# Performance work log

Hardware: AMD Instinct MI355X
Metric: run time of the kernel (lower is better)

The kernel has to match this reference:

```python
import jax, jax.numpy as jnp
import numpy as np

B, T, DIM = 4, 1024, 1024
HEADS, DH = 16, 64
MEM, CMEM, RATIO = 1024, 256, 4
KV = CMEM + MEM + T  # 2304
TOTAL_MEM = MEM + CMEM  # 1280
NEG = -np.finfo(np.float32).max


def shift(x):
    # Faithful port of the pad/flatten/reshape relative-position shift trick.
    b, h, i, j = x.shape
    x = jnp.concatenate([x, jnp.zeros((b, h, i, i), x.dtype)], axis=-1)  # [b,h,i,i+j]
    l = i + j - 1
    x = x.reshape(b, h, i * (i + j))
    pad = (-x.shape[-1]) % l
    x = jnp.pad(x, ((0, 0), (0, 0), (0, pad)))
    x = x.reshape(b, h, -1, l)
    return x[:, :, :i, i - 1:]  # [b,h,i,j]


def setup_inputs() -> dict:
    key = jax.random.key(0)
    ks = jax.random.split(key, 10)
    s = 0.02
    return {
        "x": jax.random.normal(ks[0], (B, T, DIM), jnp.float32),
        "mem": jax.random.normal(ks[1], (B, MEM, DIM), jnp.float32),
        "cmem": jax.random.normal(ks[2], (B, CMEM, DIM), jnp.float32),
        "pos_emb": jax.random.normal(ks[3], (HEADS, KV, DH), jnp.float32),
        "input_mask": jnp.ones((B, T), bool),
        "Wq": jax.random.normal(ks[4], (DIM, DIM), jnp.float32) * s,
        "Wkv": jax.random.normal(ks[5], (2 * DIM, DIM), jnp.float32) * s,
        "Wout": jax.random.normal(ks[6], (DIM, DIM), jnp.float32) * s,
        "bout": jnp.zeros((DIM,), jnp.float32),
        "conv_w": jax.random.normal(ks[7], (DIM, DIM, RATIO), jnp.float32) * s,
        "conv_b": jnp.zeros((DIM,), jnp.float32),
    }


def reference(x, mem, cmem, pos_emb, input_mask, Wq, Wkv, Wout, bout, conv_w, conv_b):
    b, t, e = x.shape
    scale = DH ** -0.5

    q = x @ Wq.T                                             # [b,t,e]
    kv_input = jnp.concatenate([cmem, mem, x], axis=1)       # [b,kv,e]
    kv_len = kv_input.shape[1]
    kv = kv_input @ Wkv.T                                    # [b,kv,2e]
    k, v = jnp.split(kv, 2, axis=-1)

    def mh(z):
        return z.reshape(z.shape[0], z.shape[1], HEADS, DH).transpose(0, 2, 1, 3)

    qh, kh, vh = mh(q), mh(k), mh(v)                         # [b,h,*,dh]

    dots = jnp.einsum('bhid,bhjd->bhij', qh, kh) * scale     # [b,h,t,kv]

    pe = pos_emb[:, -kv_len:].astype(qh.dtype)               # [h,kv,dh]
    pos_dots = shift(jnp.einsum('bhid,hjd->bhij', qh, pe) * scale)
    dots = dots + pos_dots

    # input mask (padded True over mem+cmem positions)
    m = input_mask[:, None, :, None] & input_mask[:, None, None, :]  # [b,1,t,t]
    m = jnp.pad(m, ((0, 0), (0, 0), (0, 0), (TOTAL_MEM, 0)), constant_values=True)
    dots = jnp.where(m, dots, NEG)

    # causal mask shifted by total memory length
    causal = jnp.triu(jnp.ones((t, t + TOTAL_MEM), bool), k=1 + TOTAL_MEM)
    dots = jnp.where(causal[None, None], NEG, dots)

    attn = jax.nn.softmax(dots, axis=-1)
    out = jnp.einsum('bhij,bhjd->bhid', attn, vh)
    out = out.transpose(0, 2, 1, 3).reshape(b, t, e)
    logits = out @ Wout.T + bout

    # memory update (eval path, calc_memory=True)
    queue = jnp.concatenate([mem, x], axis=1)                # [b,mem+t,e]
    new_mem = queue[:, -MEM:]
    old_mem = jax.lax.stop_gradient(queue[:, :-MEM])         # [b,t,e], t % RATIO == 0
    comp = jax.lax.conv_general_dilated(
        old_mem.transpose(0, 2, 1), conv_w, (RATIO,), 'VALID',
        dimension_numbers=('NCH', 'OIH', 'NCH')) + conv_b[None, :, None]
    comp = comp.transpose(0, 2, 1)                           # [b,t//RATIO,e]
    new_cmem = jnp.concatenate([cmem, comp], axis=1)[:, -CMEM:]

    return logits, new_mem, new_cmem
```

## Files before the change

### kernel.cpp

```cpp
#include <hip/hip_runtime.h>
#include <hip/hip_bf16.h>
#include <hip/hip_fp16.h>
#include <cstdint>
#include <cstddef>
#include <cstring>

using bf16 = __hip_bfloat16;

constexpr int TS    = 1024;
constexpr int DIM   = 1024;
constexpr int MEMN  = 1024;
constexpr int CMEMN = 256;
constexpr int KVN   = 2304;
constexpr int TMEM  = 1280;

typedef __attribute__((ext_vector_type(8))) short short8;
typedef __attribute__((ext_vector_type(4))) float f32x4;

__device__ __forceinline__ unsigned short f2bf_us(float f){
    __hip_bfloat16 t = __float2bfloat16(f);
    unsigned short us; memcpy(&us, &t, 2); return us;
}
__device__ __forceinline__ int sw8(int row){ return (row & 7) ^ ((row >> 3) & 7); }

__device__ __forceinline__ short8 ldfrag(const unsigned short* base, int row, int chunk) {
    int ch = chunk ^ sw8(row);
    return *(const short8*)(base + row*64 + ch*8);
}
__device__ __forceinline__ void gl2lds16(const void* g, void* l) {
    __builtin_amdgcn_global_load_lds(
        (const __attribute__((address_space(1))) void*)g,
        (__attribute__((address_space(3))) void*)l, 16, 0, 0);
}
__device__ __forceinline__ short8 ldg8(const unsigned short* p){ return *(const short8*)p; }

__global__ __launch_bounds__(256) void pack(
    const float* __restrict__ x, const float* __restrict__ memp,
    const float* __restrict__ cmem, const float* __restrict__ Wq,
    const float* __restrict__ Wkv, const float* __restrict__ Wout,
    const float* __restrict__ cw, const float* __restrict__ pe,
    unsigned short* __restrict__ kvin, unsigned short* __restrict__ wqb,
    unsigned short* __restrict__ wkvb, unsigned short* __restrict__ woutb,
    unsigned short* __restrict__ cw2b, unsigned short* __restrict__ peb)
{
    const size_t t8 = ((size_t)blockIdx.x * 256 + threadIdx.x) * 8;
    unsigned short h[8];
    if (t8 < 9437184) {
        size_t g = t8 >> 10;
        int cc = (int)(t8 & 1023);
        int b = (int)(g / KVN), j = (int)(g % KVN);
        const float* src;
        if (j < CMEMN)      src = cmem + ((size_t)b*CMEMN + j)*1024 + cc;
        else if (j < TMEM)  src = memp + ((size_t)b*MEMN + (j - CMEMN))*1024 + cc;
        else                src = x    + ((size_t)b*TS   + (j - TMEM))*1024 + cc;
        float4 f0 = *(const float4*)src; float4 f1 = *(const float4*)(src + 4);
        h[0]=f2bf_us(f0.x); h[1]=f2bf_us(f0.y); h[2]=f2bf_us(f0.z); h[3]=f2bf_us(f0.w);
        h[4]=f2bf_us(f1.x); h[5]=f2bf_us(f1.y); h[6]=f2bf_us(f1.z); h[7]=f2bf_us(f1.w);
        *(uint4*)(kvin + t8) = *(const uint4*)h;
    } else if (t8 < 13631488) {
        const float* src; unsigned short* dst; float sc = 1.0f;
        if (t8 < 10485760)      { src = Wq   + (t8 - 9437184);  dst = wqb   + (t8 - 9437184); sc = 0.125f; }
        else if (t8 < 12582912) { src = Wkv  + (t8 - 10485760); dst = wkvb  + (t8 - 10485760); }
        else                    { src = Wout + (t8 - 12582912); dst = woutb + (t8 - 12582912); }
        float4 f0 = *(const float4*)src; float4 f1 = *(const float4*)(src + 4);
        h[0]=f2bf_us(f0.x*sc); h[1]=f2bf_us(f0.y*sc); h[2]=f2bf_us(f0.z*sc); h[3]=f2bf_us(f0.w*sc);
        h[4]=f2bf_us(f1.x*sc); h[5]=f2bf_us(f1.y*sc); h[6]=f2bf_us(f1.z*sc); h[7]=f2bf_us(f1.w*sc);
        *(uint4*)dst = *(const uint4*)h;
    } else if (t8 < 17825792) {
        size_t o8 = t8 - 13631488;
        int o = (int)(o8 >> 12); int rem = (int)(o8 & 4095);
        int r = rem >> 10, i = rem & 1023;
        #pragma unroll
        for (int p = 0; p < 8; ++p) h[p] = f2bf_us(cw[(o << 12) + (i + p)*4 + r]);
        *(uint4*)(cw2b + o8) = *(const uint4*)h;
    } else {
        size_t o8 = t8 - 17825792;
        const float* src = pe + o8;
        float4 f0 = *(const float4*)src; float4 f1 = *(const float4*)(src + 4);
        h[0]=f2bf_us(f0.x); h[1]=f2bf_us(f0.y); h[2]=f2bf_us(f0.z); h[3]=f2bf_us(f0.w);
        h[4]=f2bf_us(f1.x); h[5]=f2bf_us(f1.y); h[6]=f2bf_us(f1.z); h[7]=f2bf_us(f1.w);
        *(uint4*)(peb + o8) = *(const uint4*)h;
    }
}

template<int EPI, int QMODE>
__global__ __launch_bounds__(256) void gemm_mfma(
    const bf16* __restrict__ Abf, const bf16* __restrict__ Bbf,
    const float* __restrict__ bias, void* __restrict__ Cptr,
    void* __restrict__ C2, int M, int N, int K)
{
    __shared__ alignas(16) unsigned short As[128*64];
    __shared__ alignas(16) unsigned short Bs[128*64];
    const int tid = threadIdx.x, lane = tid & 63, w = tid >> 6;
    const int quad = lane >> 4, colq = lane & 15;
    const int wm = w >> 1, wn = w & 1;
    const int m0 = blockIdx.x * 128, n0 = blockIdx.y * 128;
    size_t abase;
    if (QMODE == 0)      abase = (size_t)m0 * K;
    else if (QMODE == 1) abase = ((size_t)((m0 >> 10)*KVN + TMEM + (m0 & 1023))) * 1024;
    else                 abase = ((size_t)((m0 >> 8)*KVN + CMEMN)) * 1024 + (size_t)(m0 & 255) * 4096;
    const unsigned short* Ag = (const unsigned short*)Abf + abase;
    const unsigned short* Bg = (const unsigned short*)Bbf + (size_t)n0 * K;

    const int srow0 = w*32 + (lane >> 3);
    const int sch2  = lane & 7;

    f32x4 acc[4][4];
    #pragma unroll
    for (int i = 0; i < 4; ++i)
        #pragma unroll
        for (int j = 0; j < 4; ++j) acc[i][j] = (f32x4){0.f,0.f,0.f,0.f};

    for (int k0 = 0; k0 < K; k0 += 64) {
        __syncthreads();
        #pragma unroll
        for (int c = 0; c < 4; ++c) {
            int rr = srow0 + c*8;
            int ch = sch2 ^ sw8(rr);
            gl2lds16(Ag + (size_t)rr*K + k0 + ch*8, &As[(w*32 + c*8)*64]);
            gl2lds16(Bg + (size_t)rr*K + k0 + ch*8, &Bs[(w*32 + c*8)*64]);
        }
        __syncthreads();
        short8 af[4][2], bfr[4][2];
        #pragma unroll
        for (int i = 0; i < 4; ++i) {
            af[i][0]  = ldfrag(As, wm*64 + i*16 + colq, quad);
            af[i][1]  = ldfrag(As, wm*64 + i*16 + colq, 4 + quad);
            bfr[i][0] = ldfrag(Bs, wn*64 + i*16 + colq, quad);
            bfr[i][1] = ldfrag(Bs, wn*64 + i*16 + colq, 4 + quad);
        }
        #pragma unroll
        for (int i = 0; i < 4; ++i)
            #pragma unroll
            for (int j = 0; j < 4; ++j) {
                f32x4 t = __builtin_amdgcn_mfma_f32_16x16x32_bf16(af[i][0], bfr[j][0], acc[i][j], 0, 0, 0);
                acc[i][j] = __builtin_amdgcn_mfma_f32_16x16x32_bf16(af[i][1], bfr[j][1], t, 0, 0, 0);
            }
    }
    if (EPI == 2) {
        const int b = m0 / KVN;
        const int jj0 = (m0 - b*KVN) + wm*64;
        if (n0 < 1024) {
            bf16* kn = (bf16*)Cptr;
            #pragma unroll
            for (int j = 0; j < 4; ++j) {
                int col = n0 + wn*64 + j*16 + colq;
                #pragma unroll
                for (int i = 0; i < 4; ++i)
                    #pragma unroll
                    for (int r = 0; r < 4; ++r)
                        kn[(size_t)(b*KVN + jj0 + i*16 + quad*4 + r)*1024 + col] =
                            __float2bfloat16(acc[i][j][r]);
            }
        } else {
            unsigned short* vp = (unsigned short*)C2;
            #pragma unroll
            for (int j = 0; j < 4; ++j) {
                int col = n0 + wn*64 + j*16 + colq;
                int hh = (col >> 6) & 15, d = col & 63;
                #pragma unroll
                for (int i = 0; i < 4; ++i) {
                    int jjb = jj0 + i*16 + quad*4;
                    ushort4 u;
                    u.x = f2bf_us(acc[i][j][0]); u.y = f2bf_us(acc[i][j][1]);
                    u.z = f2bf_us(acc[i][j][2]); u.w = f2bf_us(acc[i][j][3]);
                    *(ushort4*)(vp + ((size_t)((b*16 + hh)*64 + d))*KVN + jjb) = u;
                }
            }
        }
    } else {
        #pragma unroll
        for (int j = 0; j < 4; ++j) {
            int col = n0 + wn*64 + j*16 + colq;
            float bj = bias ? bias[col] : 0.0f;
            #pragma unroll
            for (int i = 0; i < 4; ++i)
                #pragma unroll
                for (int r = 0; r < 4; ++r) {
                    size_t row = (size_t)(m0 + wm*64 + i*16 + quad*4 + r);
                    float v = acc[i][j][r] + bj;
                    if (EPI == 1) ((bf16*)Cptr)[row*N + col] = __float2bfloat16(v);
                    else          ((float*)Cptr)[row*N + col] = v;
                }
        }
    }
}

__global__ __launch_bounds__(256, 2) void attn(
    const unsigned short* __restrict__ qg,
    const unsigned short* __restrict__ kq,
    const unsigned short* __restrict__ vh,
    const unsigned short* __restrict__ peb,
    bf16* __restrict__ out)
{
    __shared__ alignas(16) unsigned short Kt[64*64];
    __shared__ alignas(16) unsigned short Vt[64*64];
    __shared__ alignas(16) unsigned short PEr[256*64];
    __shared__ alignas(16) unsigned short Pb[128*64];

    const int tid  = threadIdx.x;
    const int lane = tid & 63, w = tid >> 6;
    const int quad = lane >> 4, colq = lane & 15;
    const int jr = lane >> 3, l7 = lane & 7;

    const int bx = blockIdx.x;
    const int b = bx & 3, h = (bx >> 2) & 15, q0 = (bx >> 6) * 128;

    #pragma unroll
    for (int c = 0; c < 4; ++c) {
        int row = c*32 + w*8 + jr;
        gl2lds16(qg + ((size_t)(b*1024 + q0 + row))*1024 + h*64 + (l7 ^ sw8(row))*8,
                 &Pb[(c*32 + w*8)*64]);
    }
    const int c0p = 896 - q0;
    #pragma unroll
    for (int c = 0; c < 4; ++c) {
        int cg = c0p + c*32 + w*8 + jr;
        int slot = cg & 255;
        gl2lds16(peb + ((size_t)h*KVN + cg)*64 + (l7 ^ sw8(slot))*8,
                 &PEr[((c0p + c*32 + w*8) & 255)*64]);
    }
    __syncthreads();
    short8 qa[2][2];
    #pragma unroll
    for (int it2 = 0; it2 < 2; ++it2) {
        qa[it2][0] = ldfrag(Pb, 32*w + 16*it2 + colq, quad);
        qa[it2][1] = ldfrag(Pb, 32*w + 16*it2 + colq, 4 + quad);
    }

    const unsigned short* kbase = kq  + (size_t)b*KVN*1024 + h*64;
    const unsigned short* vbase = vh  + ((size_t)((b*16 + h)*64))*KVN;
    const unsigned short* pbase = peb + (size_t)h*KVN*64;

    const int row0 = w*8 + jr, row1 = 32 + w*8 + jr;
    const int ch0 = (l7 ^ sw8(row0))*8;
    const int ch1 = (l7 ^ sw8(row1))*8;

    f32x4 oacc[2][4];
    float l_[2][4];
    #pragma unroll
    for (int it2 = 0; it2 < 2; ++it2) {
        #pragma unroll
        for (int dt = 0; dt < 4; ++dt) oacc[it2][dt] = (f32x4){0.f,0.f,0.f,0.f};
        #pragma unroll
        for (int r = 0; r < 4; ++r) l_[it2][r] = 0.f;
    }
    const f32x4 zero4 = (f32x4){0.f,0.f,0.f,0.f};
    const int nkv = min(36, ((q0 + 1407) >> 6) + 1);

    short8 kr0, kr1, vr0, vr1, pr0, pr1;
    {
        kr0 = ldg8(kbase + (size_t)(row0)*1024 + ch0);
        kr1 = ldg8(kbase + (size_t)(row1)*1024 + ch1);
        vr0 = ldg8(vbase + (size_t)row0*KVN + ch0);
        vr1 = ldg8(vbase + (size_t)row1*KVN + ch1);
        int cb = 0 - q0 + 1024;
        int cg0 = cb + row0, cg1 = cb + row1;
        pr0 = ldg8(pbase + (size_t)min(cg0, KVN-1)*64 + ch0);
        pr1 = ldg8(pbase + (size_t)min(cg1, KVN-1)*64 + ch1);
    }

    for (int kvt = 0; kvt < nkv; ++kvt) {
        const int kv0 = kvt * 64;
        asm volatile("s_waitcnt lgkmcnt(0)" ::: "memory");
        __builtin_amdgcn_s_barrier();
        *(short8*)(&Kt[row0*64 + l7*8]) = kr0;
        *(short8*)(&Kt[row1*64 + l7*8]) = kr1;
        *(short8*)(&Vt[row0*64 + l7*8]) = vr0;
        *(short8*)(&Vt[row1*64 + l7*8]) = vr1;
        {
            int cb = kv0 - q0 + 1024;
            int s0 = (cb + row0) & 255, s1 = (cb + row1) & 255;
            *(short8*)(&PEr[s0*64 + l7*8]) = pr0;
            *(short8*)(&PEr[s1*64 + l7*8]) = pr1;
        }
        if (kvt + 1 < nkv) {
            int kvn = kv0 + 64;
            kr0 = ldg8(kbase + (size_t)(kvn + row0)*1024 + ch0);
            kr1 = ldg8(kbase + (size_t)(kvn + row1)*1024 + ch1);
            vr0 = ldg8(vbase + (size_t)row0*KVN + kvn + ch0);
            vr1 = ldg8(vbase + (size_t)row1*KVN + kvn + ch1);
            int cb2 = kvn - q0 + 1024;
            int cg0 = cb2 + row0, cg1 = cb2 + row1;
            pr0 = ldg8(pbase + (size_t)min(cg0, KVN-1)*64 + ch0);
            pr1 = ldg8(pbase + (size_t)min(cg1, KVN-1)*64 + ch1);
        }
        __builtin_amdgcn_sched_barrier(0);
        asm volatile("s_waitcnt lgkmcnt(0)" ::: "memory");
        __builtin_amdgcn_s_barrier();

        short8 kf[4][2], vf[4][2];
        #pragma unroll
        for (int nt = 0; nt < 4; ++nt) {
            kf[nt][0] = ldfrag(Kt, nt*16 + colq, quad);
            kf[nt][1] = ldfrag(Kt, nt*16 + colq, 4 + quad);
            vf[nt][0] = ldfrag(Vt, nt*16 + colq, quad);
            vf[nt][1] = ldfrag(Vt, nt*16 + colq, 4 + quad);
        }

        #pragma unroll
        for (int it2 = 0; it2 < 2; ++it2) {
            f32x4 facc[4];
            __builtin_amdgcn_s_setprio(1);
            #pragma unroll
            for (int nt = 0; nt < 4; ++nt) {
                f32x4 t = __builtin_amdgcn_mfma_f32_16x16x32_bf16(qa[it2][0], kf[nt][0], zero4, 0, 0, 0);
                facc[nt] = __builtin_amdgcn_mfma_f32_16x16x32_bf16(qa[it2][1], kf[nt][1], t, 0, 0, 0);
            }
            const int cb = kv0 - q0 + 1008 - 32*w - 16*it2;
            f32x4 pacc[5];
            #pragma unroll
            for (int pnt = 0; pnt < 5; ++pnt) {
                int slot = (cb + pnt*16 + colq) & 255;
                short8 b0 = ldfrag(PEr, slot, quad);
                short8 b1 = ldfrag(PEr, slot, 4 + quad);
                f32x4 t = __builtin_amdgcn_mfma_f32_16x16x32_bf16(qa[it2][0], b0, zero4, 0, 0, 0);
                pacc[pnt] = __builtin_amdgcn_mfma_f32_16x16x32_bf16(qa[it2][1], b1, t, 0, 0, 0);
            }
            __builtin_amdgcn_s_setprio(0);
            const int prow0 = 32*w + 16*it2 + 4*quad;
            #pragma unroll
            for (int r = 0; r < 4; ++r) {
                int tt = colq + 15 - 4*quad - r;
                int src = (lane & 48) | (tt & 15);
                float sh[5];
                #pragma unroll
                for (int p = 0; p < 5; ++p) sh[p] = __shfl(pacc[p][r], src, 64);
                int ig = q0 + prow0 + r;
                float lsum = 0.f;
                float ps[4];
                #pragma unroll
                for (int nt = 0; nt < 4; ++nt) {
                    float g = (tt < 16) ? sh[nt] : sh[nt + 1];
                    float v = facc[nt][r] + g;
                    int jg = kv0 + nt*16 + colq;
                    float s = (jg - ig > TMEM) ? -1e30f : v;
                    ps[nt] = __expf(s);
                    lsum += ps[nt];
                }
                l_[it2][r] += lsum;
                int prow = prow0 + r;
                int swp = sw8(prow);
                #pragma unroll
                for (int nt = 0; nt < 4; ++nt) {
                    int cc = nt*16 + colq;
                    Pb[prow*64 + (((cc >> 3) ^ swp))*8 + (cc & 7)] = f2bf_us(ps[nt]);
                }
            }
            short8 pa0 = ldfrag(Pb, 32*w + 16*it2 + colq, quad);
            short8 pa1 = ldfrag(Pb, 32*w + 16*it2 + colq, 4 + quad);
            __builtin_amdgcn_s_setprio(1);
            #pragma unroll
            for (int dt = 0; dt < 4; ++dt) {
                f32x4 t = __builtin_amdgcn_mfma_f32_16x16x32_bf16(pa0, vf[dt][0], oacc[it2][dt], 0, 0, 0);
                oacc[it2][dt] = __builtin_amdgcn_mfma_f32_16x16x32_bf16(pa1, vf[dt][1], t, 0, 0, 0);
            }
            __builtin_amdgcn_s_setprio(0);
        }
    }

    #pragma unroll
    for (int it2 = 0; it2 < 2; ++it2) {
        #pragma unroll
        for (int r = 0; r < 4; ++r) {
            float lt = l_[it2][r];
            #pragma unroll
            for (int off = 1; off < 16; off <<= 1) lt += __shfl_xor(lt, off, 64);
            float inv = 1.0f / lt;
            size_t row = (size_t)(b*1024 + q0 + 32*w + 16*it2 + 4*quad + r);
            #pragma unroll
            for (int dt = 0; dt < 4; ++dt)
                out[row*1024 + h*64 + dt*16 + colq] = __float2bfloat16(oacc[it2][dt][r] * inv);
        }
    }
}

__global__ __launch_bounds__(256) void copy_u4(const uint4* __restrict__ src,
                                               uint4* __restrict__ dst, int n)
{
    int i = blockIdx.x * 256 + threadIdx.x;
    if (i < n) dst[i] = src[i];
}

extern "C" void kernel_launch(void* const* d_in, const int* in_sizes, int n_in,
                              void* d_out, int out_size, void* d_ws, size_t ws_size,
                              hipStream_t stream)
{
    const float* x    = (const float*)d_in[0];
    const float* memp = (const float*)d_in[1];
    const float* cmem = (const float*)d_in[2];
    const float* pe   = (const float*)d_in[3];
    const float* Wq   = (const float*)d_in[5];
    const float* Wkv  = (const float*)d_in[6];
    const float* Wout = (const float*)d_in[7];
    const float* bout = (const float*)d_in[8];
    const float* cw   = (const float*)d_in[9];
    const float* cb   = (const float*)d_in[10];
    float* outp = (float*)d_out;

    char* wsb = (char*)d_ws;
    unsigned short* kvin  = (unsigned short*)(wsb);
    unsigned short* knat  = (unsigned short*)(wsb + 18874368);
    unsigned short* vhb   = (unsigned short*)(wsb + 37748736);
    unsigned short* qb    = (unsigned short*)(wsb + 56623104);
    bf16*           ao    = (bf16*)(wsb + 65011712);
    unsigned short* wqb   = (unsigned short*)(wsb + 73400320);
    unsigned short* wkvb  = (unsigned short*)(wsb + 75497472);
    unsigned short* woutb = (unsigned short*)(wsb + 79691776);
    unsigned short* cw2b  = (unsigned short*)(wsb + 81788928);
    unsigned short* peb   = (unsigned short*)(wsb + 90177536);

    pack<<<dim3(9856), 256, 0, stream>>>(x, memp, cmem, Wq, Wkv, Wout, cw, pe,
        kvin, wqb, wkvb, woutb, cw2b, peb);
    gemm_mfma<1,1><<<dim3(32, 8), 256, 0, stream>>>((const bf16*)kvin, (const bf16*)wqb,
        nullptr, qb, nullptr, 4096, 1024, 1024);
    gemm_mfma<2,0><<<dim3(72, 16), 256, 0, stream>>>((const bf16*)kvin, (const bf16*)wkvb,
        nullptr, knat, vhb, 9216, 2048, 1024);
    attn<<<dim3(512), 256, 0, stream>>>(qb, knat, vhb, peb, ao);
    gemm_mfma<0,0><<<dim3(32, 8), 256, 0, stream>>>(ao, (const bf16*)woutb,
        bout, outp, nullptr, 4096, 1024, 1024);
    copy_u4<<<dim3(4096), 256, 0, stream>>>((const uint4*)x,
        (uint4*)(outp + 4194304), 1048576);
    gemm_mfma<0,2><<<dim3(8, 8), 256, 0, stream>>>((const bf16*)kvin, (const bf16*)cw2b,
        cb, outp + 8388608, nullptr, 1024, 1024, 4096);
}
```

Measured before the change: 583.5 us.

## Double-buffer K/V via direct global-to-LDS loads and use exp2 softmax

The attention kernel now stages K, V and positional-embedding tiles straight into LDS with async global-to-LDS loads into a two-deep K/V buffer, replacing the register-staged copy. Two tiles are kept in flight and synchronised with vmcnt waits. Q fragments are loaded straight from global into registers. The softmax uses exp2 with log2(e) folded into the Wq prescale, and QK and PE MFMAs for both row groups are batched before the softmax. The Pb scratch is halved. Risks are vmcnt accounting errors, and a possible correctness problem because Pb rows are now indexed as 16*w+4*quad for both it2 iterations, so the two passes reuse the same rows.

```diff
diff --git a/kernel.cpp b/kernel.cpp
--- a/kernel.cpp
+++ b/kernel.cpp
@@ -59,7 +59,7 @@
         *(uint4*)(kvin + t8) = *(const uint4*)h;
     } else if (t8 < 13631488) {
         const float* src; unsigned short* dst; float sc = 1.0f;
-        if (t8 < 10485760)      { src = Wq   + (t8 - 9437184);  dst = wqb   + (t8 - 9437184); sc = 0.125f; }
+        if (t8 < 10485760)      { src = Wq   + (t8 - 9437184);  dst = wqb   + (t8 - 9437184); sc = 0.18033688011112043f; }
         else if (t8 < 12582912) { src = Wkv  + (t8 - 10485760); dst = wkvb  + (t8 - 10485760); }
         else                    { src = Wout + (t8 - 12582912); dst = woutb + (t8 - 12582912); }
         float4 f0 = *(const float4*)src; float4 f1 = *(const float4*)(src + 4);
@@ -193,10 +193,10 @@
     const unsigned short* __restrict__ peb,
     bf16* __restrict__ out)
 {
-    __shared__ alignas(16) unsigned short Kt[64*64];
-    __shared__ alignas(16) unsigned short Vt[64*64];
+    __shared__ alignas(16) unsigned short Kt[2][64*64];
+    __shared__ alignas(16) unsigned short Vt[2][64*64];
     __shared__ alignas(16) unsigned short PEr[256*64];
-    __shared__ alignas(16) unsigned short Pb[128*64];
+    __shared__ alignas(16) unsigned short Pb[64*64];
 
     const int tid  = threadIdx.x;
     const int lane = tid & 63, w = tid >> 6;
@@ -206,35 +206,49 @@
     const int bx = blockIdx.x;
     const int b = bx & 3, h = (bx >> 2) & 15, q0 = (bx >> 6) * 128;
 
+    const unsigned short* kbase = kq  + (size_t)b*KVN*1024 + h*64;
+    const unsigned short* vbase = vh  + ((size_t)((b*16 + h)*64))*KVN;
+    const unsigned short* pbase = peb + (size_t)h*KVN*64;
+
+    short8 qa[2][2];
     #pragma unroll
-    for (int c = 0; c < 4; ++c) {
-        int row = c*32 + w*8 + jr;
-        gl2lds16(qg + ((size_t)(b*1024 + q0 + row))*1024 + h*64 + (l7 ^ sw8(row))*8,
-                 &Pb[(c*32 + w*8)*64]);
-    }
+    for (int it2 = 0; it2 < 2; ++it2) {
+        const unsigned short* qp = qg + ((size_t)(b*1024 + q0 + 32*w + 16*it2 + colq))*1024 + h*64;
+        qa[it2][0] = ldg8(qp + quad*8);
+        qa[it2][1] = ldg8(qp + 32 + quad*8);
+    }
+    __builtin_amdgcn_sched_barrier(0);
+
+    const int row0 = w*8 + jr;
+    const int row1 = 32 + row0;
+    const int ch0 = (l7 ^ sw8(row0))*8;
+    const int ch1 = (l7 ^ sw8(row1))*8;
+
+    auto stage_kv = [&](int kv0s, int buf) {
+        gl2lds16(kbase + (size_t)(kv0s + row0)*1024 + ch0, &Kt[buf][(w*8)*64]);
+        gl2lds16(kbase + (size_t)(kv0s + row1)*1024 + ch1, &Kt[buf][(32 + w*8)*64]);
+        gl2lds16(vbase + (size_t)row0*KVN + kv0s + ch0, &Vt[buf][(w*8)*64]);
+        gl2lds16(vbase + (size_t)row1*KVN + kv0s + ch1, &Vt[buf][(32 + w*8)*64]);
+    };
+    auto stage_pe = [&](int cbase) {
+        int cg0 = cbase + row0, cg1 = cbase + row1;
+        gl2lds16(pbase + (size_t)min(cg0, KVN-1)*64 + (l7 ^ sw8(cg0 & 255))*8,
+                 &PEr[((cbase + w*8) & 255)*64]);
+        gl2lds16(pbase + (size_t)min(cg1, KVN-1)*64 + (l7 ^ sw8(cg1 & 255))*8,
+                 &PEr[((cbase + 32 + w*8) & 255)*64]);
+    };
+
     const int c0p = 896 - q0;
     #pragma unroll
     for (int c = 0; c < 4; ++c) {
         int cg = c0p + c*32 + w*8 + jr;
-        int slot = cg & 255;
-        gl2lds16(peb + ((size_t)h*KVN + cg)*64 + (l7 ^ sw8(slot))*8,
+        gl2lds16(pbase + (size_t)cg*64 + (l7 ^ sw8(cg & 255))*8,
                  &PEr[((c0p + c*32 + w*8) & 255)*64]);
     }
-    __syncthreads();
-    short8 qa[2][2];
-    #pragma unroll
-    for (int it2 = 0; it2 < 2; ++it2) {
-        qa[it2][0] = ldfrag(Pb, 32*w + 16*it2 + colq, quad);
-        qa[it2][1] = ldfrag(Pb, 32*w + 16*it2 + colq, 4 + quad);
-    }
-
-    const unsigned short* kbase = kq  + (size_t)b*KVN*1024 + h*64;
-    const unsigned short* vbase = vh  + ((size_t)((b*16 + h)*64))*KVN;
-    const unsigned short* pbase = peb + (size_t)h*KVN*64;
-
-    const int row0 = w*8 + jr, row1 = 32 + w*8 + jr;
-    const int ch0 = (l7 ^ sw8(row0))*8;
-    const int ch1 = (l7 ^ sw8(row1))*8;
+    stage_pe(1024 - q0);
+    stage_kv(0, 0);
+    stage_kv(64, 1);
+    __builtin_amdgcn_sched_barrier(0);
 
     f32x4 oacc[2][4];
     float l_[2][4];
@@ -247,95 +261,75 @@
     }
     const f32x4 zero4 = (f32x4){0.f,0.f,0.f,0.f};
     const int nkv = min(36, ((q0 + 1407) >> 6) + 1);
-
-    short8 kr0, kr1, vr0, vr1, pr0, pr1;
-    {
-        kr0 = ldg8(kbase + (size_t)(row0)*1024 + ch0);
-        kr1 = ldg8(kbase + (size_t)(row1)*1024 + ch1);
-        vr0 = ldg8(vbase + (size_t)row0*KVN + ch0);
-        vr1 = ldg8(vbase + (size_t)row1*KVN + ch1);
-        int cb = 0 - q0 + 1024;
-        int cg0 = cb + row0, cg1 = cb + row1;
-        pr0 = ldg8(pbase + (size_t)min(cg0, KVN-1)*64 + ch0);
-        pr1 = ldg8(pbase + (size_t)min(cg1, KVN-1)*64 + ch1);
-    }
+    int cur = 0;
 
     for (int kvt = 0; kvt < nkv; ++kvt) {
         const int kv0 = kvt * 64;
+        if (kvt == nkv - 1) { asm volatile("s_waitcnt vmcnt(0)" ::: "memory"); }
+        else                { asm volatile("s_waitcnt vmcnt(4)" ::: "memory"); }
+        __builtin_amdgcn_s_barrier();
+
+        const unsigned short* KtC = &Kt[cur][0];
+        const unsigned short* VtC = &Vt[cur][0];
+        short8 kf[4][2], vf[4][2];
+        #pragma unroll
+        for (int nt = 0; nt < 4; ++nt) {
+            kf[nt][0] = ldfrag(KtC, nt*16 + colq, quad);
+            kf[nt][1] = ldfrag(KtC, nt*16 + colq, 4 + quad);
+            vf[nt][0] = ldfrag(VtC, nt*16 + colq, quad);
+            vf[nt][1] = ldfrag(VtC, nt*16 + colq, 4 + quad);
+        }
         asm volatile("s_waitcnt lgkmcnt(0)" ::: "memory");
         __builtin_amdgcn_s_barrier();
-        *(short8*)(&Kt[row0*64 + l7*8]) = kr0;
-        *(short8*)(&Kt[row1*64 + l7*8]) = kr1;
-        *(short8*)(&Vt[row0*64 + l7*8]) = vr0;
-        *(short8*)(&Vt[row1*64 + l7*8]) = vr1;
-        {
-            int cb = kv0 - q0 + 1024;
-            int s0 = (cb + row0) & 255, s1 = (cb + row1) & 255;
-            *(short8*)(&PEr[s0*64 + l7*8]) = pr0;
-            *(short8*)(&PEr[s1*64 + l7*8]) = pr1;
-        }
-        if (kvt + 1 < nkv) {
-            int kvn = kv0 + 64;
-            kr0 = ldg8(kbase + (size_t)(kvn + row0)*1024 + ch0);
-            kr1 = ldg8(kbase + (size_t)(kvn + row1)*1024 + ch1);
-            vr0 = ldg8(vbase + (size_t)row0*KVN + kvn + ch0);
-            vr1 = ldg8(vbase + (size_t)row1*KVN + kvn + ch1);
-            int cb2 = kvn - q0 + 1024;
-            int cg0 = cb2 + row0, cg1 = cb2 + row1;
-            pr0 = ldg8(pbase + (size_t)min(cg0, KVN-1)*64 + ch0);
-            pr1 = ldg8(pbase + (size_t)min(cg1, KVN-1)*64 + ch1);
-        }
+
         __builtin_amdgcn_sched_barrier(0);
-        asm volatile("s_waitcnt lgkmcnt(0)" ::: "memory");
-        __builtin_amdgcn_s_barrier();
-
-        short8 kf[4][2], vf[4][2];
-        #pragma unroll
-        for (int nt = 0; nt < 4; ++nt) {
-            kf[nt][0] = ldfrag(Kt, nt*16 + colq, quad);
-            kf[nt][1] = ldfrag(Kt, nt*16 + colq, 4 + quad);
-            vf[nt][0] = ldfrag(Vt, nt*16 + colq, quad);
-            vf[nt][1] = ldfrag(Vt, nt*16 + colq, 4 + quad);
-        }
-
-        #pragma unroll
-        for (int it2 = 0; it2 < 2; ++it2) {
-            f32x4 facc[4];
-            __builtin_amdgcn_s_setprio(1);
+        if (kvt + 1 < nkv) stage_pe(kv0 + 64 - q0 + 1024);
+        if (kvt + 2 < nkv) stage_kv(kv0 + 128, cur);
+        __builtin_amdgcn_sched_barrier(0);
+
+        f32x4 facc[2][4], pacc[2][5];
+        __builtin_amdgcn_s_setprio(1);
+        #pragma unroll
+        for (int it2 = 0; it2 < 2; ++it2)
             #pragma unroll
             for (int nt = 0; nt < 4; ++nt) {
                 f32x4 t = __builtin_amdgcn_mfma_f32_16x16x32_bf16(qa[it2][0], kf[nt][0], zero4, 0, 0, 0);
-                facc[nt] = __builtin_amdgcn_mfma_f32_16x16x32_bf16(qa[it2][1], kf[nt][1], t, 0, 0, 0);
-            }
+                facc[it2][nt] = __builtin_amdgcn_mfma_f32_16x16x32_bf16(qa[it2][1], kf[nt][1], t, 0, 0, 0);
+            }
+        #pragma unroll
+        for (int it2 = 0; it2 < 2; ++it2) {
             const int cb = kv0 - q0 + 1008 - 32*w - 16*it2;
-            f32x4 pacc[5];
             #pragma unroll
             for (int pnt = 0; pnt < 5; ++pnt) {
                 int slot = (cb + pnt*16 + colq) & 255;
                 short8 b0 = ldfrag(PEr, slot, quad);
                 short8 b1 = ldfrag(PEr, slot, 4 + quad);
                 f32x4 t = __builtin_amdgcn_mfma_f32_16x16x32_bf16(qa[it2][0], b0, zero4, 0, 0, 0);
-                pacc[pnt] = __builtin_amdgcn_mfma_f32_16x16x32_bf16(qa[it2][1], b1, t, 0, 0, 0);
-            }
-            __builtin_amdgcn_s_setprio(0);
-            const int prow0 = 32*w + 16*it2 + 4*quad;
+                pacc[it2][pnt] = __builtin_amdgcn_mfma_f32_16x16x32_bf16(qa[it2][1], b1, t, 0, 0, 0);
+            }
+        }
+        __builtin_amdgcn_s_setprio(0);
+
+        #pragma unroll
+        for (int it2 = 0; it2 < 2; ++it2) {
+            const int prow0 = 16*w + 4*quad;
             #pragma unroll
             for (int r = 0; r < 4; ++r) {
                 int tt = colq + 15 - 4*quad - r;
                 int src = (lane & 48) | (tt & 15);
                 float sh[5];
                 #pragma unroll
-                for (int p = 0; p < 5; ++p) sh[p] = __shfl(pacc[p][r], src, 64);
-                int ig = q0 + prow0 + r;
+                for (int p = 0; p < 5; ++p) sh[p] = __shfl(pacc[it2][p][r], src, 64);
+                int ig = q0 + 32*w + 16*it2 + 4*quad + r;
                 float lsum = 0.f;
                 float ps[4];
                 #pragma unroll
                 for (int nt = 0; nt < 4; ++nt) {
                     float g = (tt < 16) ? sh[nt] : sh[nt + 1];
-                    float v = facc[nt][r] + g;
+                    float v = facc[it2][nt][r] + g;
                     int jg = kv0 + nt*16 + colq;
                     float s = (jg - ig > TMEM) ? -1e30f : v;
-                    ps[nt] = __expf(s);
+                    ps[nt] = __builtin_exp2f(s);
                     lsum += ps[nt];
                 }
                 l_[it2][r] += lsum;
@@ -347,8 +341,8 @@
                     Pb[prow*64 + (((cc >> 3) ^ swp))*8 + (cc & 7)] = f2bf_us(ps[nt]);
                 }
             }
-            short8 pa0 = ldfrag(Pb, 32*w + 16*it2 + colq, quad);
-            short8 pa1 = ldfrag(Pb, 32*w + 16*it2 + colq, 4 + quad);
+            short8 pa0 = ldfrag(Pb, 16*w + colq, quad);
+            short8 pa1 = ldfrag(Pb, 16*w + colq, 4 + quad);
             __builtin_amdgcn_s_setprio(1);
             #pragma unroll
             for (int dt = 0; dt < 4; ++dt) {
@@ -357,6 +351,7 @@
             }
             __builtin_amdgcn_s_setprio(0);
         }
+        cur ^= 1;
     }
 
     #pragma unroll
```

Result: faster. 523.0 us (-10.4%).
